# Kernel optimization log

Measured on AMD Instinct MI355X. Metric: run time of the kernel, lower is better.

## Reference

```python
import jax, jax.numpy as jnp
import numpy as np

N = 8_000_000   # total nodes across the batch
B = 2048        # number of graphs (segments)
L1 = 1.0 / 50.0


def _bce(p, t):
    # elementwise BCE matching torch.nn.BCELoss: logs clamped at -100
    logp = jnp.clip(jnp.log(p), -100.0)
    log1mp = jnp.clip(jnp.log1p(-p), -100.0)
    return -(t * logp + (1.0 - t) * log1mp)


def setup_inputs() -> dict:
    key = jax.random.key(0)
    k1, k2, k3, k4, k5, k6 = jax.random.split(key, 6)
    y_mus_pred = jax.random.uniform(k1, (N,), dtype=jnp.float32)
    y_mus = jax.random.uniform(k2, (N,), dtype=jnp.float32)
    y_sat_pred = jax.random.uniform(k3, (B,), dtype=jnp.float32)
    y_sat = jax.random.uniform(k4, (B,), dtype=jnp.float32)
    batch = jnp.sort(jax.random.randint(k5, (N,), 0, B, dtype=jnp.int32))
    mask = jax.random.randint(k6, (N,), 0, 2, dtype=jnp.int32)
    return {"y_mus_pred": y_mus_pred, "y_mus": y_mus,
            "y_sat_pred": y_sat_pred, "y_sat": y_sat,
            "batch": batch, "mask": mask}


def reference(y_mus_pred, y_mus, y_sat_pred, y_sat, batch, mask):
    m = mask.astype(y_mus_pred.dtype)
    # per-node BCE on masked predictions (torch: bce_mus(pred*mask, target), reduction='sum' per graph)
    bce = _bce(y_mus_pred * m, y_mus)                      # [N]
    seg_bce = jax.ops.segment_sum(bce, batch, num_segments=B)  # [B]
    seg_cnt = jax.ops.segment_sum(m, batch, num_segments=B)    # [B] = sum(mask) per graph
    per_graph = jnp.where(seg_cnt > 0, seg_bce / jnp.maximum(seg_cnt, 1.0), 0.0)
    total = per_graph.sum()
    # scalar saturation BCE (mean reduction) scaled by L1
    total = total + _bce(y_sat_pred, y_sat).mean() * jnp.asarray(L1, y_sat_pred.dtype)
    return total
```

## Files before the change

### kernel.cpp

```cpp
#include <hip/hip_runtime.h>

#define BLOCK 256

__device__ __forceinline__ float bce_elem(float p, float t) {
    float lp  = fmaxf(__logf(p), -100.0f);
    float l1p = fmaxf(__logf(1.0f - p), -100.0f);
    return -__builtin_fmaf(t, lp - l1p, l1p);
}

__device__ __forceinline__ int wave_lower_bound(const int* __restrict__ a, int n, int v) {
    const int lane = threadIdx.x & 63;
    int lo = 0, hi = n;
    while (hi - lo > 64) {
        int range  = hi - lo;
        int stride = range / 65 + 1;
        int idx    = lo + (lane + 1) * stride;
        bool lt    = (idx < hi) && (a[idx] < v);
        int  c     = __popcll(__ballot(lt));
        int  nlo   = lo + c * stride;
        int  nhi   = nlo + stride;
        if (nhi > hi) nhi = hi;
        lo = nlo; hi = nhi;
    }
    int idx = lo + lane;
    bool ge = (idx >= hi) || (a[idx] >= v);
    unsigned long long bal = __ballot(ge);
    return bal ? (lo + __ffsll(bal) - 1) : hi;
}

#define PROC(p, t, m)                                                          \
    do {                                                                       \
        float m0 = (float)(m).x, m1 = (float)(m).y,                            \
              m2 = (float)(m).z, m3 = (float)(m).w;                            \
        accb += bce_elem((p).x * m0, (t).x);  accc += m0;                      \
        accb += bce_elem((p).y * m1, (t).y);  accc += m1;                      \
        accb += bce_elem((p).z * m2, (t).z);  accc += m2;                      \
        accb += bce_elem((p).w * m3, (t).w);  accc += m3;                      \
    } while (0)

__global__ __launch_bounds__(BLOCK, 8) void seg_kernel(
    const float* __restrict__ pred, const float* __restrict__ tgt,
    const int* __restrict__ batch, const int* __restrict__ mask,
    const float* __restrict__ sat_pred, const float* __restrict__ sat_tgt,
    float* __restrict__ per_graph, int n, int Bseg)
{
    const int b   = blockIdx.x;
    const int tid = threadIdx.x;

    __shared__ int sh_bounds[2];
    const int wid = tid >> 6;
    if (wid < 2) {
        int r = wave_lower_bound(batch, n, b + wid);
        if ((tid & 63) == 0) sh_bounds[wid] = r;
    }
    __syncthreads();
    const int lo = sh_bounds[0], hi = sh_bounds[1];

    float accb = 0.0f, accc = 0.0f;

    int a0 = (lo + 3) & ~3;
    if (a0 > hi) a0 = hi;
    const int nvec = (hi - a0) >> 2;
    const int a1   = a0 + (nvec << 2);

    for (int i = lo + tid; i < a0; i += BLOCK) {
        float mf = (float)mask[i];
        accb += bce_elem(pred[i] * mf, tgt[i]);
        accc += mf;
    }

    const float4* p4 = reinterpret_cast<const float4*>(pred) + (a0 >> 2);
    const float4* t4 = reinterpret_cast<const float4*>(tgt)  + (a0 >> 2);
    const int4*   m4 = reinterpret_cast<const int4*>(mask)   + (a0 >> 2);

    if (tid < nvec) {
        float4 pa = p4[tid];
        float4 ta = t4[tid];
        int4   ma = m4[tid];
        for (int j = tid + BLOCK; j < nvec; j += BLOCK) {
            float4 pb = p4[j];
            float4 tb = t4[j];
            int4   mb = m4[j];
            __builtin_amdgcn_sched_barrier(0);
            PROC(pa, ta, ma);
            pa = pb; ta = tb; ma = mb;
        }
        PROC(pa, ta, ma);
    }

    for (int k = a1 + tid; k < hi; k += BLOCK) {
        float mf = (float)mask[k];
        accb += bce_elem(pred[k] * mf, tgt[k]);
        accc += mf;
    }

    #pragma unroll
    for (int o = 32; o > 0; o >>= 1) {
        accb += __shfl_xor(accb, o);
        accc += __shfl_xor(accc, o);
    }
    __shared__ float wb[4], wc[4];
    if ((tid & 63) == 0) { wb[tid >> 6] = accb; wc[tid >> 6] = accc; }
    __syncthreads();
    if (tid == 0) {
        float sb = wb[0] + wb[1] + wb[2] + wb[3];
        float sc = wc[0] + wc[1] + wc[2] + wc[3];
        float pg = (sc > 0.0f) ? sb / fmaxf(sc, 1.0f) : 0.0f;
        pg += bce_elem(sat_pred[b], sat_tgt[b]) * ((1.0f / 50.0f) / (float)Bseg);
        per_graph[b] = pg;
    }
}

__global__ __launch_bounds__(256) void sum_kernel(
    const float* __restrict__ per_graph, float* __restrict__ out, int Bseg)
{
    float local = 0.0f;
    for (int i = threadIdx.x; i < Bseg; i += 256) local += per_graph[i];
    #pragma unroll
    for (int o = 32; o > 0; o >>= 1) local += __shfl_xor(local, o);
    __shared__ float ws[4];
    if ((threadIdx.x & 63) == 0) ws[threadIdx.x >> 6] = local;
    __syncthreads();
    if (threadIdx.x == 0) out[0] = ws[0] + ws[1] + ws[2] + ws[3];
}

extern "C" void kernel_launch(void* const* d_in, const int* in_sizes, int n_in,
                              void* d_out, int out_size, void* d_ws, size_t ws_size,
                              hipStream_t stream) {
    const float* y_mus_pred = (const float*)d_in[0];
    const float* y_mus      = (const float*)d_in[1];
    const float* y_sat_pred = (const float*)d_in[2];
    const float* y_sat      = (const float*)d_in[3];
    const int*   batch      = (const int*)d_in[4];
    const int*   mask       = (const int*)d_in[5];

    const int n    = in_sizes[0];
    const int Bseg = in_sizes[2];

    float* per_graph = (float*)d_ws;

    seg_kernel<<<Bseg, BLOCK, 0, stream>>>(
        y_mus_pred, y_mus, batch, mask, y_sat_pred, y_sat, per_graph, n, Bseg);
    sum_kernel<<<1, 256, 0, stream>>>(per_graph, (float*)d_out, Bseg);
}
```

Before: 153.7 us.

## Process four segments per 1024-thread block and fuse final sum via last-block counter

Each block now handles four consecutive segments with 1024 threads, routing each element into one of four per-segment accumulators using the segment boundaries. The separate sum kernel is removed: a global atomic counter lets the last finishing block reduce per_graph and write the output, with a memset resetting the counter each launch. This cuts the number of blocks and binary searches and removes one kernel launch, at the cost of per-element branching, more register pressure and the old register prefetch pipeline. A 1024-thread block with launch_bounds minimum 8 blocks may also be unsatisfiable for occupancy.

```diff
diff --git a/kernel.cpp b/kernel.cpp
--- a/kernel.cpp
+++ b/kernel.cpp
@@ -1,6 +1,7 @@
 #include <hip/hip_runtime.h>
 
-#define BLOCK 256
+#define BLOCK 1024
+#define SPB   4
 
 __device__ __forceinline__ float bce_elem(float p, float t) {
     float lp  = fmaxf(__logf(p), -100.0f);
@@ -28,100 +29,139 @@
     return bal ? (lo + __ffsll(bal) - 1) : hi;
 }
 
-#define PROC(p, t, m)                                                          \
+#define ACC(e, val, mf)                                                        \
     do {                                                                       \
-        float m0 = (float)(m).x, m1 = (float)(m).y,                            \
-              m2 = (float)(m).z, m3 = (float)(m).w;                            \
-        accb += bce_elem((p).x * m0, (t).x);  accc += m0;                      \
-        accb += bce_elem((p).y * m1, (t).y);  accc += m1;                      \
-        accb += bce_elem((p).z * m2, (t).z);  accc += m2;                      \
-        accb += bce_elem((p).w * m3, (t).w);  accc += m3;                      \
+        int s_ = ((e) >= L1) + ((e) >= L2) + ((e) >= L3);                      \
+        if      (s_ == 0) { b0 += (val); c0 += (mf); }                         \
+        else if (s_ == 1) { b1 += (val); c1 += (mf); }                         \
+        else if (s_ == 2) { b2 += (val); c2 += (mf); }                         \
+        else              { b3 += (val); c3 += (mf); }                         \
     } while (0)
 
 __global__ __launch_bounds__(BLOCK, 8) void seg_kernel(
     const float* __restrict__ pred, const float* __restrict__ tgt,
     const int* __restrict__ batch, const int* __restrict__ mask,
     const float* __restrict__ sat_pred, const float* __restrict__ sat_tgt,
-    float* __restrict__ per_graph, int n, int Bseg)
+    float* __restrict__ per_graph, unsigned* __restrict__ counter,
+    float* __restrict__ out, int n, int Bseg, int nblocks)
 {
-    const int b   = blockIdx.x;
-    const int tid = threadIdx.x;
+    const int g      = blockIdx.x;
+    const int tid    = threadIdx.x;
+    const int wid    = tid >> 6;
+    const int segbase = g * SPB;
 
-    __shared__ int sh_bounds[2];
-    const int wid = tid >> 6;
-    if (wid < 2) {
-        int r = wave_lower_bound(batch, n, b + wid);
-        if ((tid & 63) == 0) sh_bounds[wid] = r;
+    __shared__ int sh_lo[SPB + 1];
+    if (wid <= SPB) {
+        int target = segbase + wid;
+        if (target > Bseg) target = Bseg;
+        int r = wave_lower_bound(batch, n, target);
+        if ((tid & 63) == 0) sh_lo[wid] = r;
     }
     __syncthreads();
-    const int lo = sh_bounds[0], hi = sh_bounds[1];
+    const int L0 = sh_lo[0], L1 = sh_lo[1], L2 = sh_lo[2],
+              L3 = sh_lo[3], L4 = sh_lo[4];
 
-    float accb = 0.0f, accc = 0.0f;
+    float b0 = 0, c0 = 0, b1 = 0, c1 = 0, b2 = 0, c2 = 0, b3 = 0, c3 = 0;
 
-    int a0 = (lo + 3) & ~3;
-    if (a0 > hi) a0 = hi;
-    const int nvec = (hi - a0) >> 2;
+    int a0 = (L0 + 3) & ~3;
+    if (a0 > L4) a0 = L4;
+    const int nvec = (L4 - a0) >> 2;
     const int a1   = a0 + (nvec << 2);
 
-    for (int i = lo + tid; i < a0; i += BLOCK) {
+    for (int i = L0 + tid; i < a0; i += BLOCK) {
         float mf = (float)mask[i];
-        accb += bce_elem(pred[i] * mf, tgt[i]);
-        accc += mf;
+        float v  = bce_elem(pred[i] * mf, tgt[i]);
+        ACC(i, v, mf);
     }
 
     const float4* p4 = reinterpret_cast<const float4*>(pred) + (a0 >> 2);
     const float4* t4 = reinterpret_cast<const float4*>(tgt)  + (a0 >> 2);
     const int4*   m4 = reinterpret_cast<const int4*>(mask)   + (a0 >> 2);
-
-    if (tid < nvec) {
-        float4 pa = p4[tid];
-        float4 ta = t4[tid];
-        int4   ma = m4[tid];
-        for (int j = tid + BLOCK; j < nvec; j += BLOCK) {
-            float4 pb = p4[j];
-            float4 tb = t4[j];
-            int4   mb = m4[j];
-            __builtin_amdgcn_sched_barrier(0);
-            PROC(pa, ta, ma);
-            pa = pb; ta = tb; ma = mb;
+    for (int v = tid; v < nvec; v += BLOCK) {
+        float4 p = p4[v];
+        float4 t = t4[v];
+        int4   m = m4[v];
+        const int e0 = a0 + (v << 2);
+        float m0 = (float)m.x, m1 = (float)m.y, m2 = (float)m.z, m3 = (float)m.w;
+        float v0 = bce_elem(p.x * m0, t.x);
+        float v1 = bce_elem(p.y * m1, t.y);
+        float v2 = bce_elem(p.z * m2, t.z);
+        float v3 = bce_elem(p.w * m3, t.w);
+        int slo = (e0 >= L1) + (e0 >= L2) + (e0 >= L3);
+        int shi = ((e0 + 3) >= L1) + ((e0 + 3) >= L2) + ((e0 + 3) >= L3);
+        if (slo == shi) {
+            float vs = (v0 + v1) + (v2 + v3);
+            float ms = (m0 + m1) + (m2 + m3);
+            if      (slo == 0) { b0 += vs; c0 += ms; }
+            else if (slo == 1) { b1 += vs; c1 += ms; }
+            else if (slo == 2) { b2 += vs; c2 += ms; }
+            else               { b3 += vs; c3 += ms; }
+        } else {
+            ACC(e0,     v0, m0);
+            ACC(e0 + 1, v1, m1);
+            ACC(e0 + 2, v2, m2);
+            ACC(e0 + 3, v3, m3);
         }
-        PROC(pa, ta, ma);
     }
 
-    for (int k = a1 + tid; k < hi; k += BLOCK) {
-        float mf = (float)mask[k];
-        accb += bce_elem(pred[k] * mf, tgt[k]);
-        accc += mf;
+    for (int i = a1 + tid; i < L4; i += BLOCK) {
+        float mf = (float)mask[i];
+        float v  = bce_elem(pred[i] * mf, tgt[i]);
+        ACC(i, v, mf);
     }
 
     #pragma unroll
     for (int o = 32; o > 0; o >>= 1) {
-        accb += __shfl_xor(accb, o);
-        accc += __shfl_xor(accc, o);
+        b0 += __shfl_xor(b0, o);  c0 += __shfl_xor(c0, o);
+        b1 += __shfl_xor(b1, o);  c1 += __shfl_xor(c1, o);
+        b2 += __shfl_xor(b2, o);  c2 += __shfl_xor(c2, o);
+        b3 += __shfl_xor(b3, o);  c3 += __shfl_xor(c3, o);
     }
-    __shared__ float wb[4], wc[4];
-    if ((tid & 63) == 0) { wb[tid >> 6] = accb; wc[tid >> 6] = accc; }
+    __shared__ float red[16][8];
+    if ((tid & 63) == 0) {
+        float* r = red[wid];
+        r[0] = b0; r[1] = c0; r[2] = b1; r[3] = c1;
+        r[4] = b2; r[5] = c2; r[6] = b3; r[7] = c3;
+    }
     __syncthreads();
-    if (tid == 0) {
-        float sb = wb[0] + wb[1] + wb[2] + wb[3];
-        float sc = wc[0] + wc[1] + wc[2] + wc[3];
-        float pg = (sc > 0.0f) ? sb / fmaxf(sc, 1.0f) : 0.0f;
-        pg += bce_elem(sat_pred[b], sat_tgt[b]) * ((1.0f / 50.0f) / (float)Bseg);
-        per_graph[b] = pg;
+    if (tid < SPB) {
+        float sbce = 0.0f, scnt = 0.0f;
+        #pragma unroll
+        for (int w = 0; w < BLOCK / 64; ++w) {
+            sbce += red[w][2 * tid];
+            scnt += red[w][2 * tid + 1];
+        }
+        const int seg = segbase + tid;
+        if (seg < Bseg) {
+            float pg = (scnt > 0.0f) ? sbce / fmaxf(scnt, 1.0f) : 0.0f;
+            pg += bce_elem(sat_pred[seg], sat_tgt[seg]) * ((1.0f / 50.0f) / (float)Bseg);
+            per_graph[seg] = pg;
+        }
     }
-}
 
-__global__ __launch_bounds__(256) void sum_kernel(
-    const float* __restrict__ per_graph, float* __restrict__ out, int Bseg)
-{
-    float local = 0.0f;
-    for (int i = threadIdx.x; i < Bseg; i += 256) local += per_graph[i];
-    #pragma unroll
-    for (int o = 32; o > 0; o >>= 1) local += __shfl_xor(local, o);
-    __shared__ float ws[4];
-    if ((threadIdx.x & 63) == 0) ws[threadIdx.x >> 6] = local;
     __syncthreads();
-    if (threadIdx.x == 0) out[0] = ws[0] + ws[1] + ws[2] + ws[3];
+    __threadfence();
+    __shared__ unsigned s_old;
+    if (tid == 0) s_old = atomicAdd(counter, 1u);
+    __syncthreads();
+    if (s_old == (unsigned)(nblocks - 1)) {
+        __threadfence();
+        float local = 0.0f;
+        for (int i = tid; i < Bseg; i += BLOCK)
+            local += __hip_atomic_load(&per_graph[i], __ATOMIC_RELAXED,
+                                       __HIP_MEMORY_SCOPE_AGENT);
+        #pragma unroll
+        for (int o = 32; o > 0; o >>= 1) local += __shfl_xor(local, o);
+        __shared__ float wsum[16];
+        if ((tid & 63) == 0) wsum[wid] = local;
+        __syncthreads();
+        if (tid == 0) {
+            float s = 0.0f;
+            #pragma unroll
+            for (int w = 0; w < BLOCK / 64; ++w) s += wsum[w];
+            out[0] = s;
+        }
+    }
 }
 
 extern "C" void kernel_launch(void* const* d_in, const int* in_sizes, int n_in,
@@ -137,9 +177,13 @@
     const int n    = in_sizes[0];
     const int Bseg = in_sizes[2];
 
-    float* per_graph = (float*)d_ws;
+    unsigned* counter   = (unsigned*)d_ws;
+    float*    per_graph = (float*)((char*)d_ws + 256);
 
-    seg_kernel<<<Bseg, BLOCK, 0, stream>>>(
-        y_mus_pred, y_mus, batch, mask, y_sat_pred, y_sat, per_graph, n, Bseg);
-    sum_kernel<<<1, 256, 0, stream>>>(per_graph, (float*)d_out, Bseg);
+    const int nblocks = (Bseg + SPB - 1) / SPB;
+
+    hipMemsetAsync(counter, 0, sizeof(unsigned), stream);
+    seg_kernel<<<nblocks, BLOCK, 0, stream>>>(
+        y_mus_pred, y_mus, batch, mask, y_sat_pred, y_sat,
+        per_graph, counter, (float*)d_out, n, Bseg, nblocks);
 }
```

Result: slower. 321.8 us (+109.4%).

## Stream segment data through LDS with async global_load_lds double buffering

Applied to the files above, without the earlier changes.

The main vector loop now uses async global-to-LDS loads (global_load_lds, 16 bytes per lane) into per-wave double-buffered shared tiles of 256 elements. Each wave prefetches its next tile while computing the current one, and explicit vmcnt waits control completion. Block size drops from 256 to 128 threads (two waves, both doing the boundary search) with a lower occupancy hint. This aims to hide memory latency better than register double buffering, but it uses more LDS, has fewer threads per segment, and relies on hand-written waitcnt ordering.

```diff
diff --git a/kernel.cpp b/kernel.cpp
--- a/kernel.cpp
+++ b/kernel.cpp
@@ -1,6 +1,15 @@
 #include <hip/hip_runtime.h>
 
-#define BLOCK 256
+#define BLOCK 128
+#define NW    2
+#define TILE  256
+
+typedef float fx4 __attribute__((ext_vector_type(4)));
+
+#define GLD16(gp, lp)                                                          \
+    __builtin_amdgcn_global_load_lds(                                          \
+        (const __attribute__((address_space(1))) void*)(uintptr_t)(gp),        \
+        (__attribute__((address_space(3))) void*)(uintptr_t)(lp), 16, 0, 0)
 
 __device__ __forceinline__ float bce_elem(float p, float t) {
     float lp  = fmaxf(__logf(p), -100.0f);
@@ -28,30 +37,21 @@
     return bal ? (lo + __ffsll(bal) - 1) : hi;
 }
 
-#define PROC(p, t, m)                                                          \
-    do {                                                                       \
-        float m0 = (float)(m).x, m1 = (float)(m).y,                            \
-              m2 = (float)(m).z, m3 = (float)(m).w;                            \
-        accb += bce_elem((p).x * m0, (t).x);  accc += m0;                      \
-        accb += bce_elem((p).y * m1, (t).y);  accc += m1;                      \
-        accb += bce_elem((p).z * m2, (t).z);  accc += m2;                      \
-        accb += bce_elem((p).w * m3, (t).w);  accc += m3;                      \
-    } while (0)
-
-__global__ __launch_bounds__(BLOCK, 8) void seg_kernel(
+__global__ __launch_bounds__(BLOCK, 4) void seg_kernel(
     const float* __restrict__ pred, const float* __restrict__ tgt,
     const int* __restrict__ batch, const int* __restrict__ mask,
     const float* __restrict__ sat_pred, const float* __restrict__ sat_tgt,
     float* __restrict__ per_graph, int n, int Bseg)
 {
-    const int b   = blockIdx.x;
-    const int tid = threadIdx.x;
+    const int b    = blockIdx.x;
+    const int tid  = threadIdx.x;
+    const int w    = tid >> 6;
+    const int lane = tid & 63;
 
     __shared__ int sh_bounds[2];
-    const int wid = tid >> 6;
-    if (wid < 2) {
-        int r = wave_lower_bound(batch, n, b + wid);
-        if ((tid & 63) == 0) sh_bounds[wid] = r;
+    {
+        int r = wave_lower_bound(batch, n, b + w);
+        if (lane == 0) sh_bounds[w] = r;
     }
     __syncthreads();
     const int lo = sh_bounds[0], hi = sh_bounds[1];
@@ -60,8 +60,8 @@
 
     int a0 = (lo + 3) & ~3;
     if (a0 > hi) a0 = hi;
-    const int nvec = (hi - a0) >> 2;
-    const int a1   = a0 + (nvec << 2);
+    const int ntiles = (hi - a0) >> 8;
+    const int a1     = a0 + (ntiles << 8);
 
     for (int i = lo + tid; i < a0; i += BLOCK) {
         float mf = (float)mask[i];
@@ -69,28 +69,53 @@
         accc += mf;
     }
 
-    const float4* p4 = reinterpret_cast<const float4*>(pred) + (a0 >> 2);
-    const float4* t4 = reinterpret_cast<const float4*>(tgt)  + (a0 >> 2);
-    const int4*   m4 = reinterpret_cast<const int4*>(mask)   + (a0 >> 2);
+    __shared__ float pb[NW][2][TILE];
+    __shared__ float tb[NW][2][TILE];
+    __shared__ int   mb[NW][2][TILE];
 
-    if (tid < nvec) {
-        float4 pa = p4[tid];
-        float4 ta = t4[tid];
-        int4   ma = m4[tid];
-        for (int j = tid + BLOCK; j < nvec; j += BLOCK) {
-            float4 pb = p4[j];
-            float4 tb = t4[j];
-            int4   mb = m4[j];
-            __builtin_amdgcn_sched_barrier(0);
-            PROC(pa, ta, ma);
-            pa = pb; ta = tb; ma = mb;
+    const float* psrc = pred + a0;
+    const float* tsrc = tgt  + a0;
+    const int*   msrc = mask + a0;
+    const int loff = lane << 2;
+
+    const int myntiles = (ntiles > w) ? ((ntiles - w + 1) >> 1) : 0;
+
+    if (myntiles > 0) {
+        const int e = (w << 8) + loff;
+        GLD16(psrc + e, &pb[w][0][0]);
+        GLD16(tsrc + e, &tb[w][0][0]);
+        GLD16(msrc + e, &mb[w][0][0]);
+    }
+    for (int j = 0; j < myntiles; ++j) {
+        const int jn = j + 1;
+        if (jn < myntiles) {
+            const int tn = w + (jn << 1);
+            const int e  = (tn << 8) + loff;
+            const int nb = jn & 1;
+            GLD16(psrc + e, &pb[w][nb][0]);
+            GLD16(tsrc + e, &tb[w][nb][0]);
+            GLD16(msrc + e, &mb[w][nb][0]);
+            asm volatile("s_waitcnt vmcnt(3)" ::: "memory");
+        } else {
+            asm volatile("s_waitcnt vmcnt(0)" ::: "memory");
         }
-        PROC(pa, ta, ma);
+        __builtin_amdgcn_sched_barrier(0);
+        const int bf = j & 1;
+        fx4 p = *(const fx4*)&pb[w][bf][loff];
+        fx4 t = *(const fx4*)&tb[w][bf][loff];
+        const int* mm = &mb[w][bf][loff];
+        float m0 = (float)mm[0], m1 = (float)mm[1],
+              m2 = (float)mm[2], m3 = (float)mm[3];
+        accb += bce_elem(p[0] * m0, t[0]);  accc += m0;
+        accb += bce_elem(p[1] * m1, t[1]);  accc += m1;
+        accb += bce_elem(p[2] * m2, t[2]);  accc += m2;
+        accb += bce_elem(p[3] * m3, t[3]);  accc += m3;
+        __builtin_amdgcn_sched_barrier(0);
     }
 
-    for (int k = a1 + tid; k < hi; k += BLOCK) {
-        float mf = (float)mask[k];
-        accb += bce_elem(pred[k] * mf, tgt[k]);
+    for (int i = a1 + tid; i < hi; i += BLOCK) {
+        float mf = (float)mask[i];
+        accb += bce_elem(pred[i] * mf, tgt[i]);
         accc += mf;
     }
 
@@ -99,12 +124,12 @@
         accb += __shfl_xor(accb, o);
         accc += __shfl_xor(accc, o);
     }
-    __shared__ float wb[4], wc[4];
-    if ((tid & 63) == 0) { wb[tid >> 6] = accb; wc[tid >> 6] = accc; }
+    __shared__ float wb[NW], wc[NW];
+    if (lane == 0) { wb[w] = accb; wc[w] = accc; }
     __syncthreads();
     if (tid == 0) {
-        float sb = wb[0] + wb[1] + wb[2] + wb[3];
-        float sc = wc[0] + wc[1] + wc[2] + wc[3];
+        float sb = wb[0] + wb[1];
+        float sc = wc[0] + wc[1];
         float pg = (sc > 0.0f) ? sb / fmaxf(sc, 1.0f) : 0.0f;
         pg += bce_elem(sat_pred[b], sat_tgt[b]) * ((1.0f / 50.0f) / (float)Bseg);
         per_graph[b] = pg;
```

Measured after the change: 153.9 us. Within noise of the previous version (+0.2%).
